# Optimization experiments

Measured on AMD Instinct MI355X. Metric: run time of the kernel, lower is better.

The kernel has to match this reference:

```python
import jax, jax.numpy as jnp
import numpy as np

D_IN = 512
EMBED = 256
N = 8192

def setup_inputs() -> dict:
    key = jax.random.key(0)
    ks = jax.random.split(key, 6)
    s_in = 1.0 / np.sqrt(D_IN)
    s_e = 1.0 / np.sqrt(EMBED)
    return {
        "X": jax.random.normal(ks[0], (N, D_IN), dtype=jnp.float32),
        "W_Q": jax.random.uniform(ks[1], (EMBED, D_IN), jnp.float32, -s_in, s_in),
        "W_K": jax.random.uniform(ks[2], (EMBED, D_IN), jnp.float32, -s_in, s_in),
        "W_V": jax.random.uniform(ks[3], (EMBED, D_IN), jnp.float32, -s_in, s_in),
        "head_w": jax.random.uniform(ks[4], (1, EMBED), jnp.float32, -s_e, s_e),
        "head_b": jax.random.uniform(ks[5], (1,), jnp.float32, -s_e, s_e),
    }

def reference(X, W_Q, W_K, W_V, head_w, head_b):
    # Projections: nn.Linear(x) = x @ W.T
    Q = X @ W_Q.T                      # [N, D]
    K = X @ W_K.T                      # [N, D]
    V = X @ W_V.T                      # [N, D]
    A = Q @ K.T                        # [N, N] unnormalized linear attention
    Z = A @ V                          # [N, D]
    preds = Z @ head_w.T + head_b      # [N, 1]
    return preds[:, 0]                 # [N]
```

## Files before the change

kernel.cpp:

```cpp
#include <hip/hip_runtime.h>

typedef unsigned long long ull;

#define D_IN 512
#define NBLK 256
#define SCALE 16777216.0f
#define INV_SCALE 5.9604644775390625e-08f
#define AG __HIP_MEMORY_SCOPE_AGENT

#define WS_TFX 0
#define WS_RFX 32768
#define WS_CNT 36864
#define WS_WVP 40960
#define N_ZERO 4616

__device__ __forceinline__ void fstore_cg(float* p, float v) {
    __hip_atomic_store((unsigned*)p, __builtin_bit_cast(unsigned, v),
                       __ATOMIC_RELAXED, AG);
}
__device__ __forceinline__ ull uload_cg(const ull* p) {
    return __hip_atomic_load(p, __ATOMIC_RELAXED, AG);
}
__device__ __forceinline__ ulonglong2 load_b128_coherent(const ull* p) {
    ulonglong2 v;
    asm volatile("global_load_dwordx4 %0, %1, off sc0 sc1\n\t"
                 "s_waitcnt vmcnt(0)"
                 : "=&v"(v) : "v"(p) : "memory");
    return v;
}

__global__ __launch_bounds__(512) void k_prep(const float* __restrict__ W_V,
                                              const float* __restrict__ head_w,
                                              float* __restrict__ wvp,
                                              ull* __restrict__ z) {
    const int j   = blockIdx.x;
    const int tid = threadIdx.x;
    float acc = 0.f;
    const int e0 = j * 32;
#pragma unroll 8
    for (int m = 0; m < 32; ++m)
        acc += head_w[e0 + m] * W_V[(size_t)(e0 + m) * D_IN + tid];
    wvp[(size_t)j * D_IN + tid] = acc;

    for (int i = j * 512 + tid; i < N_ZERO; i += 8 * 512) z[i] = 0ull;
}

__global__ __launch_bounds__(512) void k_one(
    const float* __restrict__ X,
    const float* __restrict__ W_Q,
    const float* __restrict__ W_K,
    const float* __restrict__ head_b,
    float* __restrict__ out,
    char* __restrict__ ws)
{
    ull*   t_fixed = (ull*)(ws + WS_TFX);
    ull*   r_fixed = (ull*)(ws + WS_RFX);
    ull*   cnts    = (ull*)(ws + WS_CNT);
    ull*   t_cnt   = cnts + 0;
    ull*   r_cnt   = cnts + 1;
    const float* wvp = (const float*)(ws + WS_WVP);

    const int b    = blockIdx.x;
    const int tid  = threadIdx.x;
    const int lane = tid & 63;
    const int wid  = tid >> 6;
    const int c0   = lane * 4;
    const int c1   = 256 + lane * 4;

    __shared__ float lds[8][D_IN];
    __shared__ float t_lds[D_IN];
    __shared__ float r_lds[D_IN];
    __shared__ float u_lds[8];
    __shared__ unsigned flag_s;

    float4 wv0 = {0.f,0.f,0.f,0.f}, wv1 = {0.f,0.f,0.f,0.f};
#pragma unroll
    for (int j = 0; j < 8; ++j) {
        const float4 a  = *(const float4*)(wvp + (size_t)j * D_IN + c0);
        const float4 bq = *(const float4*)(wvp + (size_t)j * D_IN + c1);
        wv0.x += a.x;  wv0.y += a.y;  wv0.z += a.z;  wv0.w += a.w;
        wv1.x += bq.x; wv1.y += bq.y; wv1.z += bq.z; wv1.w += bq.w;
    }

    float4 t0 = {0.f,0.f,0.f,0.f};
    float4 t1 = {0.f,0.f,0.f,0.f};
    const int row0 = b * 32 + wid * 4;
#pragma unroll
    for (int r = 0; r < 4; ++r) {
        const float* xr = X + (size_t)(row0 + r) * D_IN;
        const float4 a  = *(const float4*)(xr + c0);
        const float4 bq = *(const float4*)(xr + c1);
        float p = a.x*wv0.x  + a.y*wv0.y  + a.z*wv0.z  + a.w*wv0.w
                + bq.x*wv1.x + bq.y*wv1.y + bq.z*wv1.z + bq.w*wv1.w;
#pragma unroll
        for (int off = 32; off >= 1; off >>= 1) p += __shfl_xor(p, off, 64);
        t0.x += p*a.x;  t0.y += p*a.y;  t0.z += p*a.z;  t0.w += p*a.w;
        t1.x += p*bq.x; t1.y += p*bq.y; t1.z += p*bq.z; t1.w += p*bq.w;
    }
    *(float4*)(&lds[wid][c0]) = t0;
    *(float4*)(&lds[wid][c1]) = t1;
    __syncthreads();
    {
        float s = 0.f;
#pragma unroll
        for (int w = 0; w < 8; ++w) s += lds[w][tid];
        const long long v = llrintf(s * SCALE);
        ull old = atomicAdd(&t_fixed[(size_t)(b & 7) * D_IN + tid], (ull)v);
        unsigned keep = (unsigned)old ^ (unsigned)(old >> 32);
        asm volatile("" :: "v"(keep));
    }
    __syncthreads();

    if (tid == 0) flag_s = (unsigned)atomicAdd(t_cnt, 1ull);
    __syncthreads();
    const unsigned arrival = flag_s;

    if (arrival >= 224u) {
        const int k = (int)arrival - 224;
        if (tid == 0) {
            while (uload_cg(t_cnt) < 256ull) __builtin_amdgcn_s_sleep(1);
        }
        __syncthreads();

        long long acc = 0;
#pragma unroll
        for (int j = 0; j < 8; ++j)
            acc += (long long)uload_cg(&t_fixed[(size_t)j * D_IN + tid]);
        t_lds[tid] = (float)acc * INV_SCALE;
        __syncthreads();

        {
            const int e = 8 * k + wid;
            const float4 ta = *(const float4*)(t_lds + c0);
            const float4 tb = *(const float4*)(t_lds + c1);
            const float4 ka = *(const float4*)(W_K + (size_t)e * D_IN + c0);
            const float4 kb = *(const float4*)(W_K + (size_t)e * D_IN + c1);
            float p = ta.x*ka.x + ta.y*ka.y + ta.z*ka.z + ta.w*ka.w
                    + tb.x*kb.x + tb.y*kb.y + tb.z*kb.z + tb.w*kb.w;
#pragma unroll
            for (int off = 32; off >= 1; off >>= 1) p += __shfl_xor(p, off, 64);
            if (lane == 0) u_lds[wid] = p;
        }
        __syncthreads();

        {
            float racc = 0.f;
#pragma unroll
            for (int m = 0; m < 8; ++m)
                racc += u_lds[m] * W_Q[(size_t)(8 * k + m) * D_IN + tid];
            const long long v = llrintf(racc * SCALE);
            ull old = atomicAdd(&r_fixed[tid], (ull)v);
            unsigned keep = (unsigned)old ^ (unsigned)(old >> 32);
            asm volatile("" :: "v"(keep));
        }
        __syncthreads();
        if (tid == 0) atomicAdd(r_cnt, 1ull);
    }

    if (tid == 0) {
        while (uload_cg(r_cnt) < 32ull) __builtin_amdgcn_s_sleep(2);
    }
    __syncthreads();

    if (tid < 256) {
        ulonglong2 v = load_b128_coherent(r_fixed + 2 * tid);
        r_lds[2 * tid]     = (float)(long long)v.x * INV_SCALE;
        r_lds[2 * tid + 1] = (float)(long long)v.y * INV_SCALE;
    }
    __syncthreads();

    const float4 r0 = *(const float4*)(r_lds + c0);
    const float4 r1 = *(const float4*)(r_lds + c1);
    const float bb  = head_b[0];

#pragma unroll
    for (int r = 0; r < 4; ++r) {
        const float* xr = X + (size_t)(row0 + r) * D_IN;
        const float4 a  = *(const float4*)(xr + c0);
        const float4 bq = *(const float4*)(xr + c1);
        float p = a.x*r0.x  + a.y*r0.y  + a.z*r0.z  + a.w*r0.w
                + bq.x*r1.x + bq.y*r1.y + bq.z*r1.z + bq.w*r1.w;
#pragma unroll
        for (int off = 32; off >= 1; off >>= 1) p += __shfl_xor(p, off, 64);
        if (lane == 0) out[row0 + r] = p + bb;
    }
}

extern "C" void kernel_launch(void* const* d_in, const int* in_sizes, int n_in,
                              void* d_out, int out_size, void* d_ws, size_t ws_size,
                              hipStream_t stream) {
    const float* X      = (const float*)d_in[0];
    const float* W_Q    = (const float*)d_in[1];
    const float* W_K    = (const float*)d_in[2];
    const float* W_V    = (const float*)d_in[3];
    const float* head_w = (const float*)d_in[4];
    const float* head_b = (const float*)d_in[5];
    float* out = (float*)d_out;
    char* ws   = (char*)d_ws;

    float* wvp = (float*)(ws + WS_WVP);

    k_prep<<<8,    512, 0, stream>>>(W_V, head_w, wvp, (ull*)ws);
    k_one <<<NBLK, 512, 0, stream>>>(X, W_Q, W_K, head_b, out, ws);
}
```

Measured before the change: 26.25 us.

## Keep X rows in registers and fan out r via per-tail replicas

Loads each block's X rows once into registers and reuses them for both passes instead of reloading X after the grid-wide sync. The final r-vector broadcast changes: each of the 32 tail blocks writes a replica and sets its own flag, and non-tail blocks poll one replica chosen by block index rather than all blocks spinning on a single counter. W_K/W_Q rows are also touched early as a prefetch. The intent is to cut X re-read traffic and contention on one hot counter, at the cost of more registers, extra workspace and an extra flag round-trip.

After: 23.64 us. 1.11x faster.

```diff
diff --git a/kernel.cpp b/kernel.cpp
--- a/kernel.cpp
+++ b/kernel.cpp
@@ -4,15 +4,20 @@
 
 #define D_IN 512
 #define NBLK 256
+#define NTAIL 32
 #define SCALE 16777216.0f
 #define INV_SCALE 5.9604644775390625e-08f
 #define AG __HIP_MEMORY_SCOPE_AGENT
 
-#define WS_TFX 0
-#define WS_RFX 32768
-#define WS_CNT 36864
-#define WS_WVP 40960
-#define N_ZERO 4616
+#define KEEP4(v) asm volatile("" : "+v"(v.x), "+v"(v.y), "+v"(v.z), "+v"(v.w))
+
+#define WS_TFX   0
+#define WS_RFX   32768
+#define WS_CNT   36864
+#define WS_RFLAG 36928
+#define WS_RREP  40960
+#define WS_WVP   106496
+#define N_ZERO   4872
 
 __device__ __forceinline__ void fstore_cg(float* p, float v) {
     __hip_atomic_store((unsigned*)p, __builtin_bit_cast(unsigned, v),
@@ -58,6 +63,8 @@
     ull*   cnts    = (ull*)(ws + WS_CNT);
     ull*   t_cnt   = cnts + 0;
     ull*   r_cnt   = cnts + 1;
+    ull*   rflag   = (ull*)(ws + WS_RFLAG);
+    float* rrep    = (float*)(ws + WS_RREP);
     const float* wvp = (const float*)(ws + WS_WVP);
 
     const int b    = blockIdx.x;
@@ -73,6 +80,11 @@
     __shared__ float u_lds[8];
     __shared__ unsigned flag_s;
 
+    {
+        float pk = W_K[(size_t)b * 512 + tid];
+        float pq = W_Q[(size_t)b * 512 + tid];
+        asm volatile("" :: "v"(pk), "v"(pq));
+    }
     float4 wv0 = {0.f,0.f,0.f,0.f}, wv1 = {0.f,0.f,0.f,0.f};
 #pragma unroll
     for (int j = 0; j < 8; ++j) {
@@ -82,20 +94,25 @@
         wv1.x += bq.x; wv1.y += bq.y; wv1.z += bq.z; wv1.w += bq.w;
     }
 
+    float4 xa[4], xb[4];
+    const int row0 = b * 32 + wid * 4;
+#pragma unroll
+    for (int r = 0; r < 4; ++r) {
+        const float* xr = X + (size_t)(row0 + r) * D_IN;
+        xa[r] = *(const float4*)(xr + c0);
+        xb[r] = *(const float4*)(xr + c1);
+    }
+
     float4 t0 = {0.f,0.f,0.f,0.f};
     float4 t1 = {0.f,0.f,0.f,0.f};
-    const int row0 = b * 32 + wid * 4;
 #pragma unroll
     for (int r = 0; r < 4; ++r) {
-        const float* xr = X + (size_t)(row0 + r) * D_IN;
-        const float4 a  = *(const float4*)(xr + c0);
-        const float4 bq = *(const float4*)(xr + c1);
-        float p = a.x*wv0.x  + a.y*wv0.y  + a.z*wv0.z  + a.w*wv0.w
-                + bq.x*wv1.x + bq.y*wv1.y + bq.z*wv1.z + bq.w*wv1.w;
+        float p = xa[r].x*wv0.x + xa[r].y*wv0.y + xa[r].z*wv0.z + xa[r].w*wv0.w
+                + xb[r].x*wv1.x + xb[r].y*wv1.y + xb[r].z*wv1.z + xb[r].w*wv1.w;
 #pragma unroll
         for (int off = 32; off >= 1; off >>= 1) p += __shfl_xor(p, off, 64);
-        t0.x += p*a.x;  t0.y += p*a.y;  t0.z += p*a.z;  t0.w += p*a.w;
-        t1.x += p*bq.x; t1.y += p*bq.y; t1.z += p*bq.z; t1.w += p*bq.w;
+        t0.x += p*xa[r].x; t0.y += p*xa[r].y; t0.z += p*xa[r].z; t0.w += p*xa[r].w;
+        t1.x += p*xb[r].x; t1.y += p*xb[r].y; t1.z += p*xb[r].z; t1.w += p*xb[r].w;
     }
     *(float4*)(&lds[wid][c0]) = t0;
     *(float4*)(&lds[wid][c1]) = t1;
@@ -115,10 +132,10 @@
     __syncthreads();
     const unsigned arrival = flag_s;
 
-    if (arrival >= 224u) {
-        const int k = (int)arrival - 224;
+    if (arrival >= (unsigned)(NBLK - NTAIL)) {
+        const int k = (int)arrival - (NBLK - NTAIL);
         if (tid == 0) {
-            while (uload_cg(t_cnt) < 256ull) __builtin_amdgcn_s_sleep(1);
+            while (uload_cg(t_cnt) < (ull)NBLK) __builtin_amdgcn_s_sleep(4);
         }
         __syncthreads();
 
@@ -155,31 +172,48 @@
         }
         __syncthreads();
         if (tid == 0) atomicAdd(r_cnt, 1ull);
-    }
-
-    if (tid == 0) {
-        while (uload_cg(r_cnt) < 32ull) __builtin_amdgcn_s_sleep(2);
-    }
-    __syncthreads();
-
-    if (tid < 256) {
-        ulonglong2 v = load_b128_coherent(r_fixed + 2 * tid);
-        r_lds[2 * tid]     = (float)(long long)v.x * INV_SCALE;
-        r_lds[2 * tid + 1] = (float)(long long)v.y * INV_SCALE;
-    }
-    __syncthreads();
-
+
+        if (tid == 0) {
+            while (uload_cg(r_cnt) < (ull)NTAIL) __builtin_amdgcn_s_sleep(1);
+        }
+        __syncthreads();
+        {
+            ull v = uload_cg(&r_fixed[tid]);
+            float f = (float)(long long)v * INV_SCALE;
+            r_lds[tid] = f;
+            fstore_cg(&rrep[(size_t)k * D_IN + tid], f);
+        }
+        __syncthreads();
+        if (tid == 0) atomicAdd(&rflag[(size_t)k * 8], 1ull);
+        __syncthreads();
+    } else {
+        const int rep = b & 31;
+        if (tid == 0) {
+            while (uload_cg(&rflag[(size_t)rep * 8]) == 0ull)
+                __builtin_amdgcn_s_sleep(2);
+        }
+        __syncthreads();
+        if (tid < 128) {
+            ulonglong2 v = load_b128_coherent(
+                (const ull*)(rrep + (size_t)rep * D_IN + tid * 4));
+            r_lds[tid*4+0] = __builtin_bit_cast(float, (unsigned)v.x);
+            r_lds[tid*4+1] = __builtin_bit_cast(float, (unsigned)(v.x >> 32));
+            r_lds[tid*4+2] = __builtin_bit_cast(float, (unsigned)v.y);
+            r_lds[tid*4+3] = __builtin_bit_cast(float, (unsigned)(v.y >> 32));
+        }
+        __syncthreads();
+    }
+
+#pragma unroll
+    for (int r = 0; r < 4; ++r) { KEEP4(xa[r]); KEEP4(xb[r]); }
     const float4 r0 = *(const float4*)(r_lds + c0);
     const float4 r1 = *(const float4*)(r_lds + c1);
     const float bb  = head_b[0];
 
 #pragma unroll
     for (int r = 0; r < 4; ++r) {
-        const float* xr = X + (size_t)(row0 + r) * D_IN;
-        const float4 a  = *(const float4*)(xr + c0);
-        const float4 bq = *(const float4*)(xr + c1);
-        float p = a.x*r0.x  + a.y*r0.y  + a.z*r0.z  + a.w*r0.w
-                + bq.x*r1.x + bq.y*r1.y + bq.z*r1.z + bq.w*r1.w;
+        float p = xa[r].x*r0.x + xa[r].y*r0.y + xa[r].z*r0.z + xa[r].w*r0.w
+                + xb[r].x*r1.x + xb[r].y*r1.y + xb[r].z*r1.z + xb[r].w*r1.w;
 #pragma unroll
         for (int off = 32; off >= 1; off >>= 1) p += __shfl_xor(p, off, 64);
         if (lane == 0) out[row0 + r] = p + bb;
```
